# Performance work log

Hardware: AMD Instinct MI355X
Metric: run time of the kernel (lower is better)

The kernel has to match this reference:

```python
import jax, jax.numpy as jnp
import numpy as np

B, O, M, H, E = 32, 64, 128, 4, 64  # batch, num_obj, memory_len, heads, embed


def setup_inputs() -> dict:
    key = jax.random.key(0)
    ks = jax.random.split(key, 10)
    s = 1.0 / np.sqrt(E)
    return {
        "query": jax.random.normal(ks[0], (B, O, E), jnp.float32),
        "context": jax.random.normal(ks[1], (B, M, E), jnp.float32),
        "memory": jax.random.normal(ks[2], (B, M, E), jnp.float32),
        "W_ch": jax.random.normal(ks[3], (E, H * E), jnp.float32) * s,
        "b_ch": jax.random.normal(ks[4], (H * E,), jnp.float32) * s,
        "w_logit": jax.random.normal(ks[5], (E,), jnp.float32) * s,
        "b_logit": jax.random.normal(ks[6], (1,), jnp.float32) * s,
        "W_rh": jax.random.normal(ks[7], (H * E, E), jnp.float32) * (1.0 / np.sqrt(H * E)),
        "b_rh": jax.random.normal(ks[8], (E,), jnp.float32) * (1.0 / np.sqrt(H * E)),
        "temp": jnp.float32(1.0),
    }


def reference(query, context, memory, W_ch, b_ch, w_logit, b_logit, W_rh, b_rh, temp):
    # create heads: [B,O,E] -> [B,O,H,E]
    q = (query @ W_ch + b_ch).reshape(B, O, H, E)
    # broadcast add query heads and context over memory axis: [B,O,M,H,E]
    qc = jnp.tanh(context[:, None, :, None, :] + q[:, :, None, :, :])
    # logit projection -> [B,O,M,H]
    logits = jnp.einsum("bomhe,e->bomh", qc, w_logit) + b_logit[0]
    # softmax over memory axis (dim=2)
    probs = jax.nn.softmax(logits / temp, axis=2)
    # weighted sum of memory over M: [B,O,H,E]
    heads = jnp.einsum("bomh,bme->bohe", probs, memory)
    heads = jax.nn.leaky_relu(heads, negative_slope=0.01)
    out = heads.reshape(B, O, H * E) @ W_rh + b_rh
    return out
```

## Files before the change

kernel.cpp:

```cpp
#include <hip/hip_runtime.h>
#include <hip/hip_fp16.h>

#define B 32
#define O 64
#define M 128
#define H 4
#define E 64
#define CW 66
#define SC  2.88539008177792681f
#define LOG2E 1.44269504088896341f

#if __has_builtin(__builtin_amdgcn_exp2f)
#define EXP2F(x) __builtin_amdgcn_exp2f(x)
#else
#define EXP2F(x) __exp2f(x)
#endif

__device__ __forceinline__ float rl(float v, int lane) {
    return __uint_as_float(__builtin_amdgcn_readlane(__float_as_uint(v), lane));
}

__global__ __launch_bounds__(256) void attn_kernel(
    const float* __restrict__ query,
    const float* __restrict__ context,
    const float* __restrict__ memory,
    const float* __restrict__ W_ch,
    const float* __restrict__ b_ch,
    const float* __restrict__ w_logit,
    const float* __restrict__ b_logit,
    const float* __restrict__ W_rh,
    const float* __restrict__ b_rh,
    const float* __restrict__ temp,
    float* __restrict__ out)
{
    const int t    = threadIdx.x;
    const int lane = t & 63;
    const int w    = t >> 6;
    const int bo   = blockIdx.x;
    const int b    = bo >> 6;

    __shared__ __half2 s_ctxT[E * CW];
    __shared__ float   s_red[256];

    const float* ctx = context + b * (M * E);
    {
        int e0 = 4 * (t >> 4);
        int cb = t & 15;
        #pragma unroll
        for (int pq = 0; pq < 4; ++pq) {
            int col = cb + 16 * pq;
            int m0  = 2 * col;
            float4 r0 = *(const float4*)(ctx + m0 * E + e0);
            float4 r1 = *(const float4*)(ctx + (m0 + 1) * E + e0);
            __half2 h0, h1, h2, h3;
            h0.x = __float2half_rn(r0.x * SC); h0.y = __float2half_rn(r1.x * SC);
            h1.x = __float2half_rn(r0.y * SC); h1.y = __float2half_rn(r1.y * SC);
            h2.x = __float2half_rn(r0.z * SC); h2.y = __float2half_rn(r1.z * SC);
            h3.x = __float2half_rn(r0.w * SC); h3.y = __float2half_rn(r1.w * SC);
            s_ctxT[(e0 + 0) * CW + col] = h0;
            s_ctxT[(e0 + 1) * CW + col] = h1;
            s_ctxT[(e0 + 2) * CW + col] = h2;
            s_ctxT[(e0 + 3) * CW + col] = h3;
        }
    }

    float qv;
    {
        float qq  = query[bo * E + lane];
        float acc = b_ch[t];
        const float* Wc = W_ch + w * 64 + lane;
        #pragma unroll 16
        for (int k = 0; k < 64; ++k)
            acc = fmaf(rl(qq, k), Wc[k * 256], acc);
        qv = acc * SC;
    }
    float wlv = w_logit[lane];

    __syncthreads();

    float acc0 = 0.f, acc1 = 0.f;
    #pragma unroll 8
    for (int e = 0; e < 64; ++e) {
        __half2 c2 = s_ctxT[e * CW + lane];
        float2 cf  = __half22float2(c2);
        float qe   = rl(qv, e);
        float we   = rl(wlv, e);
        float ex0  = EXP2F(cf.x + qe);
        float ex1  = EXP2F(cf.y + qe);
        float r0   = __builtin_amdgcn_rcpf(ex0 + 1.0f);
        float r1   = __builtin_amdgcn_rcpf(ex1 + 1.0f);
        acc0 = fmaf(fmaf(-2.0f, r0, 1.0f), we, acc0);
        acc1 = fmaf(fmaf(-2.0f, r1, 1.0f), we, acc1);
    }

    const float bl  = b_logit[0];
    const float lsc = (1.0f / temp[0]) * LOG2E;
    float l0 = (acc0 + bl) * lsc;
    float l1 = (acc1 + bl) * lsc;
    float mx = fmaxf(l0, l1);
    #pragma unroll
    for (int s = 1; s < 64; s <<= 1)
        mx = fmaxf(mx, __shfl_xor(mx, s));
    float e0v = EXP2F(l0 - mx);
    float e1v = EXP2F(l1 - mx);
    float sum = e0v + e1v;
    #pragma unroll
    for (int s = 1; s < 64; s <<= 1)
        sum += __shfl_xor(sum, s);
    float rs = __builtin_amdgcn_rcpf(sum);

    float hacc = 0.f;
    {
        const float* mem = memory + b * (M * E) + lane;
        #pragma unroll 8
        for (int mh = 0; mh < 64; ++mh) {
            float pe = rl(e0v, mh);
            float po = rl(e1v, mh);
            hacc = fmaf(pe, mem[(2 * mh) * E], hacc);
            hacc = fmaf(po, mem[(2 * mh + 1) * E], hacc);
        }
    }
    hacc *= rs;
    float hv = (hacc > 0.f) ? hacc : 0.01f * hacc;

    {
        float pacc = 0.f;
        const float* Wr = W_rh + (w * 64) * 64 + lane;
        #pragma unroll 16
        for (int j = 0; j < 64; ++j)
            pacc = fmaf(rl(hv, j), Wr[j * 64], pacc);
        s_red[t] = pacc;
    }
    __syncthreads();
    if (t < 64) {
        float o = s_red[t] + s_red[t + 64] + s_red[t + 128] + s_red[t + 192] + b_rh[t];
        out[bo * 64 + t] = o;
    }
}

extern "C" void kernel_launch(void* const* d_in, const int* in_sizes, int n_in,
                              void* d_out, int out_size, void* d_ws, size_t ws_size,
                              hipStream_t stream) {
    const float* query   = (const float*)d_in[0];
    const float* context = (const float*)d_in[1];
    const float* memory  = (const float*)d_in[2];
    const float* W_ch    = (const float*)d_in[3];
    const float* b_ch    = (const float*)d_in[4];
    const float* w_logit = (const float*)d_in[5];
    const float* b_logit = (const float*)d_in[6];
    const float* W_rh    = (const float*)d_in[7];
    const float* b_rh    = (const float*)d_in[8];
    const float* temp    = (const float*)d_in[9];
    float* out = (float*)d_out;

    attn_kernel<<<B * O, 256, 0, stream>>>(query, context, memory, W_ch, b_ch,
                                           w_logit, b_logit, W_rh, b_rh, temp, out);
}
```

Baseline: 110.0 us.

## Split fused attention kernel into prep, main, and output-projection kernels

Splits the single fused kernel into three. A prep kernel transposes context to fp16 once per batch, converts memory to fp16 and batches the query-head projection. The main kernel stages the fp16 context and memory into LDS, uses tanh = 1 - 2/(1+exp) with the w_logit sum folded in, and does the memory-weighted sum from LDS across all heads. A separate kernel then applies the output projection to fp16 heads. This removes the per-block redundant transposes and the uncoalesced strided memory reads, at the cost of two extra launches, workspace round trips and more fp16 rounding of memory and heads.

```diff
diff --git a/kernel.cpp b/kernel.cpp
--- a/kernel.cpp
+++ b/kernel.cpp
@@ -6,8 +6,7 @@
 #define M 128
 #define H 4
 #define E 64
-#define CW 66
-#define SC  2.88539008177792681f
+#define SC 2.88539008177792681f
 #define LOG2E 1.44269504088896341f
 
 #if __has_builtin(__builtin_amdgcn_exp2f)
@@ -19,123 +18,180 @@
 __device__ __forceinline__ float rl(float v, int lane) {
     return __uint_as_float(__builtin_amdgcn_readlane(__float_as_uint(v), lane));
 }
-
-__global__ __launch_bounds__(256) void attn_kernel(
-    const float* __restrict__ query,
-    const float* __restrict__ context,
-    const float* __restrict__ memory,
-    const float* __restrict__ W_ch,
+__device__ __forceinline__ unsigned pk2h(float a, float b) {
+    return (unsigned)__half_as_ushort(__float2half_rn(a)) |
+           ((unsigned)__half_as_ushort(__float2half_rn(b)) << 16);
+}
+
+__global__ __launch_bounds__(256) void prep_kernel(
+    const float* __restrict__ query, const float* __restrict__ context,
+    const float* __restrict__ memory, const float* __restrict__ W_ch,
     const float* __restrict__ b_ch,
-    const float* __restrict__ w_logit,
-    const float* __restrict__ b_logit,
-    const float* __restrict__ W_rh,
-    const float* __restrict__ b_rh,
-    const float* __restrict__ temp,
-    float* __restrict__ out)
+    __half* __restrict__ ctx_T, __half* __restrict__ mem_h, float* __restrict__ q_all)
 {
-    const int t    = threadIdx.x;
-    const int lane = t & 63;
-    const int w    = t >> 6;
-    const int bo   = blockIdx.x;
-    const int b    = bo >> 6;
-
-    __shared__ __half2 s_ctxT[E * CW];
-    __shared__ float   s_red[256];
-
-    const float* ctx = context + b * (M * E);
+    __shared__ float s[128 * 68];
+    const int t = threadIdx.x, blk = blockIdx.x;
+
+    if (blk < 32) {
+        const int b = blk;
+        const float* ctx = context + b * (M * E);
+        #pragma unroll
+        for (int i = 0; i < 8; ++i) {
+            int idx = i * 1024 + t * 4;
+            float4 v = *(const float4*)(ctx + idx);
+            int m = idx >> 6, e = idx & 63;
+            *(float4*)(&s[m * 68 + e]) = v;
+        }
+        {
+            const float* mem = memory + b * (M * E);
+            __half* mh = mem_h + (size_t)b * (M * E);
+            #pragma unroll
+            for (int i = 0; i < 8; ++i) {
+                int idx = i * 1024 + t * 4;
+                float4 v = *(const float4*)(mem + idx);
+                *(uint2*)(mh + idx) = make_uint2(pk2h(v.x, v.y), pk2h(v.z, v.w));
+            }
+        }
+        __syncthreads();
+        {
+            int e = t >> 2, mb = (t & 3) * 32;
+            uint4 o[4];
+            #pragma unroll
+            for (int qd = 0; qd < 4; ++qd) {
+                unsigned u[4];
+                #pragma unroll
+                for (int k = 0; k < 4; ++k) {
+                    int m0 = mb + qd * 8 + 2 * k;
+                    u[k] = pk2h(s[m0 * 68 + e] * SC, s[(m0 + 1) * 68 + e] * SC);
+                }
+                o[qd] = make_uint4(u[0], u[1], u[2], u[3]);
+            }
+            uint4* dst = (uint4*)(ctx_T + (size_t)b * (E * M) + e * M + mb);
+            dst[0] = o[0]; dst[1] = o[1]; dst[2] = o[2]; dst[3] = o[3];
+        }
+    } else {
+        const int r0 = (blk - 32) * 4;
+        s[t] = query[(r0 + (t & 3)) * 64 + (t >> 2)];
+        __syncthreads();
+        float bc = b_ch[t];
+        float a0 = bc, a1 = bc, a2 = bc, a3 = bc;
+        #pragma unroll 8
+        for (int k = 0; k < 64; ++k) {
+            float4 qv = *(const float4*)(&s[k * 4]);
+            float wv = W_ch[k * 256 + t];
+            a0 = fmaf(qv.x, wv, a0);
+            a1 = fmaf(qv.y, wv, a1);
+            a2 = fmaf(qv.z, wv, a2);
+            a3 = fmaf(qv.w, wv, a3);
+        }
+        float* qa = q_all + (size_t)r0 * 256 + t;
+        qa[0] = a0 * SC; qa[256] = a1 * SC; qa[512] = a2 * SC; qa[768] = a3 * SC;
+    }
+}
+
+__global__ __launch_bounds__(256) void attn_main(
+    const __half* __restrict__ ctx_T, const __half* __restrict__ mem_h,
+    const float* __restrict__ q_all, const float* __restrict__ w_logit,
+    const float* __restrict__ b_logit, const float* __restrict__ temp,
+    __half* __restrict__ heads_h)
+{
+    __shared__ __half s_ctx[E * M];
+    __shared__ __half s_mem[M * E];
+    __shared__ float  s_prob[M * H];
+    __shared__ float  s_part[H * 4 * E];
+
+    const int t = threadIdx.x, lane = t & 63, w = t >> 6;
+    const int bo = blockIdx.x, b = bo >> 6;
+
     {
-        int e0 = 4 * (t >> 4);
-        int cb = t & 15;
+        const uint4* g1 = (const uint4*)(ctx_T + (size_t)b * (E * M));
+        const uint4* g2 = (const uint4*)(mem_h + (size_t)b * (M * E));
+        uint4* l1 = (uint4*)s_ctx;
+        uint4* l2 = (uint4*)s_mem;
         #pragma unroll
-        for (int pq = 0; pq < 4; ++pq) {
-            int col = cb + 16 * pq;
-            int m0  = 2 * col;
-            float4 r0 = *(const float4*)(ctx + m0 * E + e0);
-            float4 r1 = *(const float4*)(ctx + (m0 + 1) * E + e0);
-            __half2 h0, h1, h2, h3;
-            h0.x = __float2half_rn(r0.x * SC); h0.y = __float2half_rn(r1.x * SC);
-            h1.x = __float2half_rn(r0.y * SC); h1.y = __float2half_rn(r1.y * SC);
-            h2.x = __float2half_rn(r0.z * SC); h2.y = __float2half_rn(r1.z * SC);
-            h3.x = __float2half_rn(r0.w * SC); h3.y = __float2half_rn(r1.w * SC);
-            s_ctxT[(e0 + 0) * CW + col] = h0;
-            s_ctxT[(e0 + 1) * CW + col] = h1;
-            s_ctxT[(e0 + 2) * CW + col] = h2;
-            s_ctxT[(e0 + 3) * CW + col] = h3;
-        }
-    }
-
-    float qv;
-    {
-        float qq  = query[bo * E + lane];
-        float acc = b_ch[t];
-        const float* Wc = W_ch + w * 64 + lane;
-        #pragma unroll 16
-        for (int k = 0; k < 64; ++k)
-            acc = fmaf(rl(qq, k), Wc[k * 256], acc);
-        qv = acc * SC;
-    }
-    float wlv = w_logit[lane];
-
+        for (int p = 0; p < 4; ++p) {
+            l1[p * 256 + t] = g1[p * 256 + t];
+            l2[p * 256 + t] = g2[p * 256 + t];
+        }
+    }
+    float qv  = q_all[bo * 256 + t];
+    float wl  = w_logit[lane];
+    float we2 = 2.0f * wl;
+    float sumw = wl;
+    #pragma unroll
+    for (int sft = 1; sft < 64; sft <<= 1) sumw += __shfl_xor(sumw, sft);
+    const float bl  = b_logit[0];
+    const float lsc = LOG2E / temp[0];
     __syncthreads();
 
     float acc0 = 0.f, acc1 = 0.f;
+    const __half2* c2p = (const __half2*)s_ctx;
     #pragma unroll 8
     for (int e = 0; e < 64; ++e) {
-        __half2 c2 = s_ctxT[e * CW + lane];
-        float2 cf  = __half22float2(c2);
-        float qe   = rl(qv, e);
-        float we   = rl(wlv, e);
-        float ex0  = EXP2F(cf.x + qe);
-        float ex1  = EXP2F(cf.y + qe);
-        float r0   = __builtin_amdgcn_rcpf(ex0 + 1.0f);
-        float r1   = __builtin_amdgcn_rcpf(ex1 + 1.0f);
-        acc0 = fmaf(fmaf(-2.0f, r0, 1.0f), we, acc0);
-        acc1 = fmaf(fmaf(-2.0f, r1, 1.0f), we, acc1);
-    }
-
-    const float bl  = b_logit[0];
-    const float lsc = (1.0f / temp[0]) * LOG2E;
-    float l0 = (acc0 + bl) * lsc;
-    float l1 = (acc1 + bl) * lsc;
+        float2 cf = __half22float2(c2p[e * 64 + lane]);
+        float qe = rl(qv, e);
+        float w2 = rl(we2, e);
+        float r0 = __builtin_amdgcn_rcpf(1.0f + EXP2F(cf.x + qe));
+        float r1 = __builtin_amdgcn_rcpf(1.0f + EXP2F(cf.y + qe));
+        acc0 = fmaf(w2, r0, acc0);
+        acc1 = fmaf(w2, r1, acc1);
+    }
+    float l0 = (sumw - acc0 + bl) * lsc;
+    float l1 = (sumw - acc1 + bl) * lsc;
     float mx = fmaxf(l0, l1);
     #pragma unroll
-    for (int s = 1; s < 64; s <<= 1)
-        mx = fmaxf(mx, __shfl_xor(mx, s));
-    float e0v = EXP2F(l0 - mx);
-    float e1v = EXP2F(l1 - mx);
-    float sum = e0v + e1v;
+    for (int sft = 1; sft < 64; sft <<= 1) mx = fmaxf(mx, __shfl_xor(mx, sft));
+    float e0 = EXP2F(l0 - mx);
+    float e1 = EXP2F(l1 - mx);
+    float sum = e0 + e1;
     #pragma unroll
-    for (int s = 1; s < 64; s <<= 1)
-        sum += __shfl_xor(sum, s);
+    for (int sft = 1; sft < 64; sft <<= 1) sum += __shfl_xor(sum, sft);
     float rs = __builtin_amdgcn_rcpf(sum);
-
-    float hacc = 0.f;
-    {
-        const float* mem = memory + b * (M * E) + lane;
-        #pragma unroll 8
-        for (int mh = 0; mh < 64; ++mh) {
-            float pe = rl(e0v, mh);
-            float po = rl(e1v, mh);
-            hacc = fmaf(pe, mem[(2 * mh) * E], hacc);
-            hacc = fmaf(po, mem[(2 * mh + 1) * E], hacc);
-        }
-    }
-    hacc *= rs;
-    float hv = (hacc > 0.f) ? hacc : 0.01f * hacc;
-
-    {
-        float pacc = 0.f;
-        const float* Wr = W_rh + (w * 64) * 64 + lane;
-        #pragma unroll 16
-        for (int j = 0; j < 64; ++j)
-            pacc = fmaf(rl(hv, j), Wr[j * 64], pacc);
-        s_red[t] = pacc;
-    }
-    __syncthreads();
-    if (t < 64) {
-        float o = s_red[t] + s_red[t + 64] + s_red[t + 128] + s_red[t + 192] + b_rh[t];
-        out[bo * 64 + t] = o;
-    }
+    s_prob[(2 * lane) * H + w]     = e0 * rs;
+    s_prob[(2 * lane + 1) * H + w] = e1 * rs;
+    __syncthreads();
+
+    float h0 = 0.f, h1 = 0.f, h2 = 0.f, h3 = 0.f;
+    #pragma unroll 8
+    for (int i = 0; i < 32; ++i) {
+        int m = 32 * w + i;
+        float4 p = *(const float4*)(&s_prob[m * 4]);
+        float mv = __half2float(s_mem[m * 64 + lane]);
+        h0 = fmaf(p.x, mv, h0);
+        h1 = fmaf(p.y, mv, h1);
+        h2 = fmaf(p.z, mv, h2);
+        h3 = fmaf(p.w, mv, h3);
+    }
+    s_part[0 * 256 + w * 64 + lane] = h0;
+    s_part[1 * 256 + w * 64 + lane] = h1;
+    s_part[2 * 256 + w * 64 + lane] = h2;
+    s_part[3 * 256 + w * 64 + lane] = h3;
+    __syncthreads();
+    float hv = s_part[w * 256 + lane] + s_part[w * 256 + 64 + lane]
+             + s_part[w * 256 + 128 + lane] + s_part[w * 256 + 192 + lane];
+    hv = (hv > 0.f) ? hv : 0.01f * hv;
+    heads_h[(size_t)bo * 256 + t] = __float2half_rn(hv);
+}
+
+__global__ __launch_bounds__(512) void post_kernel(
+    const __half* __restrict__ heads_h, const float* __restrict__ W_rh,
+    const float* __restrict__ b_rh, float* __restrict__ out)
+{
+    __shared__ __half s_h[8 * 256];
+    const int t = threadIdx.x, lane = t & 63, r = t >> 6;
+    const int r0 = blockIdx.x * 8;
+    ((uint2*)s_h)[t] = ((const uint2*)(heads_h + (size_t)r0 * 256))[t];
+    __syncthreads();
+    const __half2* hr = (const __half2*)(s_h + r * 256);
+    const float* Wp = W_rh + lane;
+    float acc = 0.f;
+    #pragma unroll 8
+    for (int jp = 0; jp < 128; ++jp) {
+        float2 hh = __half22float2(hr[jp]);
+        acc = fmaf(hh.x, Wp[(2 * jp) * 64], acc);
+        acc = fmaf(hh.y, Wp[(2 * jp + 1) * 64], acc);
+    }
+    out[(size_t)(r0 + r) * 64 + lane] = acc + b_rh[lane];
 }
 
 extern "C" void kernel_launch(void* const* d_in, const int* in_sizes, int n_in,
@@ -153,6 +209,14 @@
     const float* temp    = (const float*)d_in[9];
     float* out = (float*)d_out;
 
-    attn_kernel<<<B * O, 256, 0, stream>>>(query, context, memory, W_ch, b_ch,
-                                           w_logit, b_logit, W_rh, b_rh, temp, out);
-}
+    __half* ctx_T   = (__half*)d_ws;
+    __half* mem_h   = ctx_T + (size_t)B * E * M;
+    float*  q_all   = (float*)(mem_h + (size_t)B * M * E);
+    __half* heads_h = (__half*)(q_all + (size_t)B * O * H * E);
+
+    prep_kernel<<<544, 256, 0, stream>>>(query, context, memory, W_ch, b_ch,
+                                         ctx_T, mem_h, q_all);
+    attn_main<<<B * O, 256, 0, stream>>>(ctx_T, mem_h, q_all, w_logit,
+                                         b_logit, temp, heads_h);
+    post_kernel<<<256, 512, 0, stream>>>(heads_h, W_rh, b_rh, out);
+}
```

After: 106.7 us. -3.0%, faster.
